# Optimization experiments

Measured on AMD Instinct MI355X. Metric: run time of the kernel, lower is better.

The kernel has to match this reference:

```python
import jax, jax.numpy as jnp
import numpy as np

V, E, H, O, L = 32000, 512, 512, 32, 2
B, T = 64, 512


def setup_inputs() -> dict:
    key = jax.random.key(0)
    ks = jax.random.split(key, 10)
    s = 0.02
    x = jax.random.randint(ks[0], (B, T), 0, V, dtype=jnp.int64)
    seq_lens = jax.random.randint(ks[1], (B,), 1, T + 1, dtype=jnp.int64)
    emb = jax.random.normal(ks[2], (V, E), dtype=jnp.float32) * s
    Whx = jax.random.normal(ks[3], (L, H, E), dtype=jnp.float32) * s  # [out,in] like nn.Linear
    Whh = jax.random.normal(ks[4], (L, H, H), dtype=jnp.float32) * s
    b_h = jnp.zeros((L, H), dtype=jnp.float32)
    Wyh = jax.random.normal(ks[5], (L, H, H), dtype=jnp.float32) * s
    b_y = jnp.zeros((L, H), dtype=jnp.float32)
    Wf = jax.random.normal(ks[6], (O, H), dtype=jnp.float32) * s
    bf = jnp.zeros((O,), dtype=jnp.float32)
    return {"x": x, "sequence_lengths": seq_lens, "emb": emb, "Whx": Whx,
            "Whh": Whh, "b_h": b_h, "Wyh": Wyh, "b_y": b_y, "Wf": Wf, "bf": bf}


def reference(x, sequence_lengths, emb, Whx, Whh, b_h, Wyh, b_y, Wf, bf):
    Bsz, Tlen = x.shape
    x_emb = emb[x]                      # [B,T,E]
    xs = jnp.swapaxes(x_emb, 0, 1)      # time-major [T,B,E]
    h0 = jnp.zeros((L, Bsz, H), dtype=x_emb.dtype)

    def step(h, xt):
        inp = xt
        hs = []
        for l in range(L):
            hl = jnp.tanh(inp @ Whx[l].T + h[l] @ Whh[l].T + b_h[l])
            hs.append(hl)
            inp = hl
        # only the last layer's y is kept by the original loop
        y = inp @ Wyh[L - 1].T + b_y[L - 1]
        return jnp.stack(hs), y

    _, outputs = jax.lax.scan(step, h0, xs)     # outputs: [T,B,H]
    outputs = jnp.swapaxes(outputs, 0, 1)       # [B,T,H]
    idx = sequence_lengths - 1                  # last valid timestep per example
    final_hidden = outputs[jnp.arange(Bsz), idx]  # [B,H]
    return final_hidden @ Wf.T + bf             # [B,O]
```

## Files before the change

kernel.cpp:

```cpp
#include <hip/hip_runtime.h>

namespace {
constexpr int E_ = 512;
constexpr int H_ = 512;
constexpr int O_ = 32;
constexpr int B_ = 64;
constexpr int T_ = 512;
constexpr int RING = 8;
constexpr int FPAD = 16;
constexpr size_t H0_OFF   = 0;
constexpr size_t H1_OFF   = (size_t)RING * B_ * H_;
constexpr size_t HF_OFF   = 2 * H1_OFF;
constexpr size_t FLAG_OFF = HF_OFF + (size_t)B_ * H_;
constexpr size_t FLAG_UINTS = 8u * 32u * FPAD;
constexpr size_t WS_REQUIRED = (FLAG_OFF + FLAG_UINTS) * 4;
}

typedef float f32x4 __attribute__((ext_vector_type(4)));

__device__ __forceinline__ void coh_ld2k(const float* p, f32x4& a, f32x4& b) {
    asm volatile(
        "global_load_dwordx4 %0, %2, off sc0 sc1\n\t"
        "global_load_dwordx4 %1, %2, off offset:1024 sc0 sc1\n\t"
        "s_waitcnt vmcnt(0)"
        : "=&v"(a), "=&v"(b) : "v"(p) : "memory");
}
__device__ __forceinline__ void coh_ld4k(const float* p, const float* q,
                                         f32x4& a, f32x4& b, f32x4& c, f32x4& d) {
    asm volatile(
        "global_load_dwordx4 %0, %4, off sc0 sc1\n\t"
        "global_load_dwordx4 %1, %4, off offset:1024 sc0 sc1\n\t"
        "global_load_dwordx4 %2, %5, off sc0 sc1\n\t"
        "global_load_dwordx4 %3, %5, off offset:1024 sc0 sc1\n\t"
        "s_waitcnt vmcnt(0)"
        : "=&v"(a), "=&v"(b), "=&v"(c), "=&v"(d) : "v"(p), "v"(q) : "memory");
}
__device__ __forceinline__ unsigned flag_poll(const unsigned* p) {
    unsigned v;
    asm volatile("global_load_dword %0, %1, off sc0 sc1\n\ts_waitcnt vmcnt(0)"
                 : "=&v"(v) : "v"(p) : "memory");
    return v;
}
__device__ __forceinline__ void coh_store_u(float* p, unsigned v) {
    asm volatile("global_store_dword %0, %1, off sc0 sc1" :: "v"(p), "v"(v) : "memory");
}
__device__ __forceinline__ void flag_store(unsigned* p, unsigned v) {
    asm volatile("global_store_dword %0, %1, off sc0 sc1" :: "v"(p), "v"(v) : "memory");
}

__device__ __forceinline__ float fast_tanh(float x) {
    float e = __builtin_amdgcn_exp2f(x * 2.885390081777927f);
    return 1.0f - 2.0f * __builtin_amdgcn_rcpf(e + 1.0f);
}

__device__ __forceinline__ float reduce4(const float v[4], int lane) {
    float a[2];
#pragma unroll
    for (int j = 0; j < 2; ++j) {
        const int sel = lane & 1;
        const float mine = sel ? v[2 * j + 1] : v[2 * j];
        const float send = sel ? v[2 * j] : v[2 * j + 1];
        a[j] = mine + __shfl_xor(send, 1, 64);
    }
    const int sel = (lane >> 1) & 1;
    const float mine = sel ? a[1] : a[0];
    const float send = sel ? a[0] : a[1];
    float s = mine + __shfl_xor(send, 2, 64);
    s += __shfl_xor(s, 4, 64);
    s += __shfl_xor(s, 8, 64);
    s += __shfl_xor(s, 16, 64);
    s += __shfl_xor(s, 32, 64);
    return s;
}

__global__ __launch_bounds__(512, 4) void rnn_pipe11(
    const int* __restrict__ x, const int* __restrict__ seq_lens,
    const float* __restrict__ emb,
    const float* __restrict__ Whx, const float* __restrict__ Whh,
    const float* __restrict__ b_h,
    float* __restrict__ h0_ring, float* __restrict__ h1_ring,
    float* __restrict__ h1_final, unsigned* __restrict__ flags)
{
    const int bid   = blockIdx.x;
    const int layer = bid >> 8;
    const int g     = (bid >> 5) & 7;
    const int c     = bid & 31;
    const int tid   = threadIdx.x;
    const int wid   = tid >> 6;
    const int lane  = tid & 63;
    const int we    = wid >> 2;
    const int wr    = wid & 3;
    const int rowbase = c * 16 + wr * 4;
    const int eg0   = g * 8 + we * 4;

    __shared__ float smem[12288];
    float* const sxA = smem;
    float* const sxB = smem + 4096;
    float* const sh  = smem + 8192;
    float* const sh1 = smem;

    const float* WxL = Whx + (size_t)layer * H_ * E_;
    const float* WhL = Whh + (size_t)layer * H_ * H_;
    f32x4 wx0[4], wx1[4], wh0[4], wh1[4];
#pragma unroll
    for (int r = 0; r < 4; ++r) {
        const int row = rowbase + r;
        wx0[r] = *(const f32x4*)(WxL + (size_t)row * E_ + (lane << 2));
        wx1[r] = *(const f32x4*)(WxL + (size_t)row * E_ + 256 + (lane << 2));
        wh0[r] = *(const f32x4*)(WhL + (size_t)row * H_ + (lane << 2));
        wh1[r] = *(const f32x4*)(WhL + (size_t)row * H_ + 256 + (lane << 2));
    }
    const float bias = b_h[layer * H_ + rowbase + (lane & 3)];

    int sl4[4];
#pragma unroll
    for (int q = 0; q < 4; ++q) sl4[q] = seq_lens[eg0 + q];
    int Tg = 1;
#pragma unroll
    for (int j = 0; j < 8; ++j) {
        const int s = seq_lens[g * 8 + j];
        Tg = s > Tg ? s : Tg;
    }

    unsigned* const myflag = flags + ((size_t)(g * 32 + c)) * FPAD;
    const unsigned* const bp = flags + ((size_t)(g * 32 + (lane & 31))) * FPAD;

    const int se  = wid;
    const int seg = g * 8 + se;

    long budget = 1l << 22;

    if (layer == 0) {
        {
            const int tok = x[(size_t)seg * T_];
            *(f32x4*)&sxA[(se << 9) + (lane << 2)] =
                *(const f32x4*)(emb + ((size_t)tok << 9) + (lane << 2));
            *(f32x4*)&sxA[(se << 9) + 256 + (lane << 2)] =
                *(const f32x4*)(emb + ((size_t)tok << 9) + 256 + (lane << 2));
        }
        __syncthreads();

        for (int t = 0; t < Tg; ++t) {
            const int cur = t & 1, slot = t & 7, pslot = (t - 1) & 7;
            float* const sxc = cur ? sxB : sxA;
            float* const sxn = cur ? sxA : sxB;
            const unsigned em_prev = (((t - 1) >> 3) & 1) ? 0xFFFFFFFFu : 0u;
            const unsigned em_cur  = ((t >> 3) & 1) ? 0xFFFFFFFFu : 0u;

            if (wid == 0 && t >= RING) {
                const int tgt = t - 7;
                for (;;) {
                    const unsigned v = flag_poll(bp);
                    const bool bad = (lane < 32) && ((int)v < tgt);
                    if (!__any(bad)) break;
                    if (--budget < 0) break;
                }
            }

            if (t > 0) {
                const float* src = h0_ring + (((size_t)pslot << 6) + seg) * 512 + (lane << 2);
                f32x4 da, db;
                for (;;) {
                    f32x4 a, b;
                    coh_ld2k(src, a, b);
                    unsigned o = 0;
#pragma unroll
                    for (int m = 0; m < 4; ++m) {
                        unsigned u = __float_as_uint(a[m]) ^ em_prev; o |= u; da[m] = __uint_as_float(u);
                        unsigned w = __float_as_uint(b[m]) ^ em_prev; o |= w; db[m] = __uint_as_float(w);
                    }
                    if (!__any((o >> 30) & 1)) break;
                    if (--budget < 0) break;
                }
                *(f32x4*)&sh[(se << 9) + (lane << 2)] = da;
                *(f32x4*)&sh[(se << 9) + 256 + (lane << 2)] = db;
            } else {
                f32x4 z = 0;
                *(f32x4*)&sh[(se << 9) + (lane << 2)] = z;
                *(f32x4*)&sh[(se << 9) + 256 + (lane << 2)] = z;
            }
            f32x4 px0, px1;
            const bool havepf = (t + 1 < Tg);
            if (havepf) {
                const int tok = x[(size_t)seg * T_ + t + 1];
                px0 = *(const f32x4*)(emb + ((size_t)tok << 9) + (lane << 2));
                px1 = *(const f32x4*)(emb + ((size_t)tok << 9) + 256 + (lane << 2));
            }
            __syncthreads();

#pragma unroll
            for (int q = 0; q < 4; ++q) {
                unsigned uenc = em_cur;
                if (t < sl4[q]) {
                    const int el = (we << 2) + q;
                    const f32x4 lx0 = *(const f32x4*)&sxc[(el << 9) + (lane << 2)];
                    const f32x4 lx1 = *(const f32x4*)&sxc[(el << 9) + 256 + (lane << 2)];
                    const f32x4 h0a = *(const f32x4*)&sh[(el << 9) + (lane << 2)];
                    const f32x4 h0b = *(const f32x4*)&sh[(el << 9) + 256 + (lane << 2)];
                    float vv[4];
#pragma unroll
                    for (int r = 0; r < 4; ++r) {
                        float s = wx0[r][0] * lx0[0];
                        s = fmaf(wx0[r][1], lx0[1], s);
                        s = fmaf(wx0[r][2], lx0[2], s);
                        s = fmaf(wx0[r][3], lx0[3], s);
                        s = fmaf(wx1[r][0], lx1[0], s);
                        s = fmaf(wx1[r][1], lx1[1], s);
                        s = fmaf(wx1[r][2], lx1[2], s);
                        s = fmaf(wx1[r][3], lx1[3], s);
                        s = fmaf(wh0[r][0], h0a[0], s);
                        s = fmaf(wh0[r][1], h0a[1], s);
                        s = fmaf(wh0[r][2], h0a[2], s);
                        s = fmaf(wh0[r][3], h0a[3], s);
                        s = fmaf(wh1[r][0], h0b[0], s);
                        s = fmaf(wh1[r][1], h0b[1], s);
                        s = fmaf(wh1[r][2], h0b[2], s);
                        s = fmaf(wh1[r][3], h0b[3], s);
                        vv[r] = s;
                    }
                    const float sum = reduce4(vv, lane);
                    const float hv = fast_tanh(sum + bias);
                    uenc = __float_as_uint(hv) ^ em_cur;
                }
                if (lane < 4)
                    coh_store_u(h0_ring + (((size_t)slot << 6) + eg0 + q) * 512 + rowbase + lane, uenc);
            }
            if (havepf) {
                *(f32x4*)&sxn[(se << 9) + (lane << 2)] = px0;
                *(f32x4*)&sxn[(se << 9) + 256 + (lane << 2)] = px1;
            }
            __syncthreads();
        }
    } else {
        for (int t = 0; t < Tg; ++t) {
            const int slot = t & 7, pslot = (t - 1) & 7;
            const unsigned em0 = ((t >> 3) & 1) ? 0xFFFFFFFFu : 0u;
            const unsigned em1 = (((t - 1) >> 3) & 1) ? 0xFFFFFFFFu : 0u;

            const float* p0 = h0_ring + (((size_t)slot << 6) + seg) * 512 + (lane << 2);
            if (t > 0) {
                const float* p1 = h1_ring + (((size_t)pslot << 6) + seg) * 512 + (lane << 2);
                f32x4 d0a, d0b, d1a, d1b;
                for (;;) {
                    f32x4 a, b, c2, d2;
                    coh_ld4k(p0, p1, a, b, c2, d2);
                    unsigned o = 0;
#pragma unroll
                    for (int m = 0; m < 4; ++m) {
                        unsigned u0 = __float_as_uint(a[m])  ^ em0; o |= u0; d0a[m] = __uint_as_float(u0);
                        unsigned u1 = __float_as_uint(b[m])  ^ em0; o |= u1; d0b[m] = __uint_as_float(u1);
                        unsigned u2 = __float_as_uint(c2[m]) ^ em1; o |= u2; d1a[m] = __uint_as_float(u2);
                        unsigned u3 = __float_as_uint(d2[m]) ^ em1; o |= u3; d1b[m] = __uint_as_float(u3);
                    }
                    if (!__any((o >> 30) & 1)) break;
                    if (--budget < 0) break;
                }
                *(f32x4*)&sh[(se << 9) + (lane << 2)] = d0a;
                *(f32x4*)&sh[(se << 9) + 256 + (lane << 2)] = d0b;
                *(f32x4*)&sh1[(se << 9) + (lane << 2)] = d1a;
                *(f32x4*)&sh1[(se << 9) + 256 + (lane << 2)] = d1b;
            } else {
                f32x4 d0a, d0b;
                for (;;) {
                    f32x4 a, b;
                    coh_ld2k(p0, a, b);
                    unsigned o = 0;
#pragma unroll
                    for (int m = 0; m < 4; ++m) {
                        unsigned u0 = __float_as_uint(a[m]) ^ em0; o |= u0; d0a[m] = __uint_as_float(u0);
                        unsigned u1 = __float_as_uint(b[m]) ^ em0; o |= u1; d0b[m] = __uint_as_float(u1);
                    }
                    if (!__any((o >> 30) & 1)) break;
                    if (--budget < 0) break;
                }
                *(f32x4*)&sh[(se << 9) + (lane << 2)] = d0a;
                *(f32x4*)&sh[(se << 9) + 256 + (lane << 2)] = d0b;
                f32x4 z = 0;
                *(f32x4*)&sh1[(se << 9) + (lane << 2)] = z;
                *(f32x4*)&sh1[(se << 9) + 256 + (lane << 2)] = z;
            }
            __syncthreads();
            if (tid == 0) flag_store(myflag, (unsigned)(t + 1));

#pragma unroll
            for (int q = 0; q < 4; ++q) {
                unsigned uenc = em0;
                const bool live = (t < sl4[q]);
                float hv = 0.f;
                if (live) {
                    const int el = (we << 2) + q;
                    const f32x4 xa = *(const f32x4*)&sh[(el << 9) + (lane << 2)];
                    const f32x4 xb = *(const f32x4*)&sh[(el << 9) + 256 + (lane << 2)];
                    const f32x4 ha = *(const f32x4*)&sh1[(el << 9) + (lane << 2)];
                    const f32x4 hb = *(const f32x4*)&sh1[(el << 9) + 256 + (lane << 2)];
                    float vv[4];
#pragma unroll
                    for (int r = 0; r < 4; ++r) {
                        float s = wx0[r][0] * xa[0];
                        s = fmaf(wx0[r][1], xa[1], s);
                        s = fmaf(wx0[r][2], xa[2], s);
                        s = fmaf(wx0[r][3], xa[3], s);
                        s = fmaf(wx1[r][0], xb[0], s);
                        s = fmaf(wx1[r][1], xb[1], s);
                        s = fmaf(wx1[r][2], xb[2], s);
                        s = fmaf(wx1[r][3], xb[3], s);
                        s = fmaf(wh0[r][0], ha[0], s);
                        s = fmaf(wh0[r][1], ha[1], s);
                        s = fmaf(wh0[r][2], ha[2], s);
                        s = fmaf(wh0[r][3], ha[3], s);
                        s = fmaf(wh1[r][0], hb[0], s);
                        s = fmaf(wh1[r][1], hb[1], s);
                        s = fmaf(wh1[r][2], hb[2], s);
                        s = fmaf(wh1[r][3], hb[3], s);
                        vv[r] = s;
                    }
                    const float sum = reduce4(vv, lane);
                    hv = fast_tanh(sum + bias);
                    uenc = __float_as_uint(hv) ^ em0;
                }
                if (lane < 4) {
                    coh_store_u(h1_ring + (((size_t)slot << 6) + eg0 + q) * 512 + rowbase + lane, uenc);
                    if (live && t == sl4[q] - 1)
                        h1_final[((size_t)(eg0 + q) << 9) + rowbase + lane] = hv;
                }
            }
            __syncthreads();
        }
    }
}

__device__ __forceinline__ float dot4(float4 a, float4 b) {
    return fmaf(a.x, b.x, fmaf(a.y, b.y, fmaf(a.z, b.z, a.w * b.w)));
}
__device__ __forceinline__ float wave_reduce(float acc) {
#pragma unroll
    for (int off = 32; off > 0; off >>= 1) acc += __shfl_down(acc, off, 64);
    return acc;
}

__global__ __launch_bounds__(512) void head_kernel(
    const float* __restrict__ h1f, const float* __restrict__ Wyh,
    const float* __restrict__ b_y, const float* __restrict__ Wf,
    const float* __restrict__ bf, float* __restrict__ out)
{
    const int e = blockIdx.x;
    const int tid = threadIdx.x, wid = tid >> 6, lane = tid & 63;
    const int k0 = lane << 3;
    __shared__ float sh[H_];
    __shared__ float sy[H_];
    sh[tid] = h1f[(size_t)e * H_ + tid];
    __syncthreads();
    const float4 hA = *(const float4*)&sh[k0];
    const float4 hB = *(const float4*)&sh[k0 + 4];
    const float* Wy1 = Wyh + H_ * H_;
#pragma unroll 4
    for (int rr = 0; rr < 64; ++rr) {
        const int row = (wid << 6) + rr;
        float acc = wave_reduce(dot4(*(const float4*)&Wy1[(size_t)row * H_ + k0], hA) +
                                dot4(*(const float4*)&Wy1[(size_t)row * H_ + k0 + 4], hB));
        if (lane == 0) sy[row] = acc + b_y[H_ + row];
    }
    __syncthreads();
    const float4 yA = *(const float4*)&sy[k0];
    const float4 yB = *(const float4*)&sy[k0 + 4];
#pragma unroll
    for (int rr = 0; rr < 4; ++rr) {
        const int o = (wid << 2) + rr;
        float acc = wave_reduce(dot4(*(const float4*)&Wf[(size_t)o * H_ + k0], yA) +
                                dot4(*(const float4*)&Wf[(size_t)o * H_ + k0 + 4], yB));
        if (lane == 0) out[(size_t)e * O_ + o] = acc + bf[o];
    }
}

__global__ __launch_bounds__(1024, 1) void rnn_fused_fb(
    const int* __restrict__ x, const int* __restrict__ seq_lens,
    const float* __restrict__ emb, const float* __restrict__ Whx,
    const float* __restrict__ Whh, const float* __restrict__ b_h,
    const float* __restrict__ Wyh, const float* __restrict__ b_y,
    const float* __restrict__ Wf, const float* __restrict__ bf,
    float* __restrict__ out)
{
    const int b = blockIdx.x, tid = threadIdx.x;
    const int wave = tid >> 6, lane = tid & 63, k0 = lane << 3;
    __shared__ float s_inp[E_];
    __shared__ float s_h0[2][H_];
    __shared__ float s_h1[2][H_];
    __shared__ float s_y[H_];
    if (tid < H_) { s_h0[0][tid]=0.f; s_h0[1][tid]=0.f; s_h1[0][tid]=0.f; s_h1[1][tid]=0.f; }
    const int Tb = seq_lens[b];
    const float* Whx0 = Whx; const float* Whx1 = Whx + H_*E_;
    const float* Whh0 = Whh; const float* Whh1 = Whh + H_*H_;
    for (int t = 0; t < Tb; ++t) {
        const int cur = t & 1, prv = cur ^ 1;
        if (tid < E_) { const int tok = x[b*T_+t]; s_inp[tid] = emb[(size_t)tok*E_+tid]; }
        __syncthreads();
        const float4 iA = *(const float4*)&s_inp[k0], iB = *(const float4*)&s_inp[k0+4];
        const float4 pA = *(const float4*)&s_h0[prv][k0], pB = *(const float4*)&s_h0[prv][k0+4];
#pragma unroll 4
        for (int r = 0; r < 32; ++r) {
            const int i = (wave<<5)+r;
            float acc = dot4(*(const float4*)&Whx0[i*E_+k0], iA) + dot4(*(const float4*)&Whx0[i*E_+k0+4], iB)
                      + dot4(*(const float4*)&Whh0[i*H_+k0], pA) + dot4(*(const float4*)&Whh0[i*H_+k0+4], pB);
            acc = wave_reduce(acc);
            if (lane == 0) s_h0[cur][i] = tanhf(acc + b_h[i]);
        }
        __syncthreads();
        const float4 cA = *(const float4*)&s_h0[cur][k0], cB = *(const float4*)&s_h0[cur][k0+4];
        const float4 qA = *(const float4*)&s_h1[prv][k0], qB = *(const float4*)&s_h1[prv][k0+4];
#pragma unroll 4
        for (int r = 0; r < 32; ++r) {
            const int i = (wave<<5)+r;
            float acc = dot4(*(const float4*)&Whx1[i*E_+k0], cA) + dot4(*(const float4*)&Whx1[i*E_+k0+4], cB)
                      + dot4(*(const float4*)&Whh1[i*H_+k0], qA) + dot4(*(const float4*)&Whh1[i*H_+k0+4], qB);
            acc = wave_reduce(acc);
            if (lane == 0) s_h1[cur][i] = tanhf(acc + b_h[H_+i]);
        }
        __syncthreads();
    }
    const int lastb = (Tb-1) & 1;
    const float4 hA = *(const float4*)&s_h1[lastb][k0], hB = *(const float4*)&s_h1[lastb][k0+4];
    const float* Wy1 = Wyh + H_*H_;
#pragma unroll 4
    for (int r = 0; r < 32; ++r) {
        const int i = (wave<<5)+r;
        float acc = wave_reduce(dot4(*(const float4*)&Wy1[i*H_+k0], hA) + dot4(*(const float4*)&Wy1[i*H_+k0+4], hB));
        if (lane == 0) s_y[i] = acc + b_y[H_+i];
    }
    __syncthreads();
    const float4 yA = *(const float4*)&s_y[k0], yB = *(const float4*)&s_y[k0+4];
    if (wave < 8) {
#pragma unroll
        for (int r = 0; r < 4; ++r) {
            const int o = (wave<<2)+r;
            float acc = wave_reduce(dot4(*(const float4*)&Wf[o*H_+k0], yA) + dot4(*(const float4*)&Wf[o*H_+k0+4], yB));
            if (lane == 0) out[b*O_+o] = acc + bf[o];
        }
    }
}

extern "C" void kernel_launch(void* const* d_in, const int* in_sizes, int n_in,
                              void* d_out, int out_size, void* d_ws, size_t ws_size,
                              hipStream_t stream) {
    const int*   x    = (const int*)d_in[0];
    const int*   sl   = (const int*)d_in[1];
    const float* emb  = (const float*)d_in[2];
    const float* Whx  = (const float*)d_in[3];
    const float* Whh  = (const float*)d_in[4];
    const float* b_h  = (const float*)d_in[5];
    const float* Wyh  = (const float*)d_in[6];
    const float* b_y  = (const float*)d_in[7];
    const float* Wf   = (const float*)d_in[8];
    const float* bf   = (const float*)d_in[9];
    float* out = (float*)d_out;

    if (ws_size < WS_REQUIRED) {
        rnn_fused_fb<<<B_, 1024, 0, stream>>>(x, sl, emb, Whx, Whh, b_h, Wyh, b_y, Wf, bf, out);
        return;
    }

    float* ws_f = (float*)d_ws;
    float* h0_ring = ws_f + H0_OFF;
    float* h1_ring = ws_f + H1_OFF;
    float* h1f     = ws_f + HF_OFF;
    unsigned* flags = (unsigned*)(ws_f + FLAG_OFF);

    hipMemsetAsync(h0_ring, 0xFF, 2 * H1_OFF * sizeof(float), stream);
    hipMemsetAsync(flags, 0, FLAG_UINTS * sizeof(unsigned), stream);
    rnn_pipe11<<<512, 512, 0, stream>>>(x, sl, emb, Whx, Whh, b_h,
                                        h0_ring, h1_ring, h1f, flags);
    head_kernel<<<B_, 512, 0, stream>>>(h1f, Wyh, b_y, Wf, bf, out);
}
```

Baseline: 1.941 ms.

## Sort batch by sequence length so groups share similar trip counts

Adds a small rank kernel that computes a permutation of batch elements sorted by descending sequence length. The recurrent kernel then assigns sorted examples to groups of eight, so each group's loop bound (the max length in the group) tracks its members closely and short groups exit early. This removes timesteps that were computed only because one long sequence sat in an otherwise short group. It costs an extra tiny kernel launch and an indirect lookup for tokens and final-state writes.

```diff
diff --git a/kernel.cpp b/kernel.cpp
--- a/kernel.cpp
+++ b/kernel.cpp
@@ -13,7 +13,8 @@
 constexpr size_t HF_OFF   = 2 * H1_OFF;
 constexpr size_t FLAG_OFF = HF_OFF + (size_t)B_ * H_;
 constexpr size_t FLAG_UINTS = 8u * 32u * FPAD;
-constexpr size_t WS_REQUIRED = (FLAG_OFF + FLAG_UINTS) * 4;
+constexpr size_t PERM_OFF = FLAG_OFF + FLAG_UINTS;
+constexpr size_t WS_REQUIRED = (PERM_OFF + 64) * 4;
 }
 
 typedef float f32x4 __attribute__((ext_vector_type(4)));
@@ -73,13 +74,25 @@
     return s;
 }
 
-__global__ __launch_bounds__(512, 4) void rnn_pipe11(
+__global__ void rank_kernel(const int* __restrict__ sl, int* __restrict__ perm) {
+    const int e = threadIdx.x;
+    const int my = sl[e];
+    int rank = 0;
+    for (int j = 0; j < B_; ++j) {
+        const int o = sl[j];
+        rank += (o > my) || (o == my && j < e);
+    }
+    perm[rank] = e;
+}
+
+__global__ __launch_bounds__(512, 4) void rnn_pipe12(
     const int* __restrict__ x, const int* __restrict__ seq_lens,
     const float* __restrict__ emb,
     const float* __restrict__ Whx, const float* __restrict__ Whh,
     const float* __restrict__ b_h,
     float* __restrict__ h0_ring, float* __restrict__ h1_ring,
-    float* __restrict__ h1_final, unsigned* __restrict__ flags)
+    float* __restrict__ h1_final, unsigned* __restrict__ flags,
+    const int* __restrict__ perm)
 {
     const int bid   = blockIdx.x;
     const int layer = bid >> 8;
@@ -112,13 +125,16 @@
     }
     const float bias = b_h[layer * H_ + rowbase + (lane & 3)];
 
-    int sl4[4];
-#pragma unroll
-    for (int q = 0; q < 4; ++q) sl4[q] = seq_lens[eg0 + q];
+    int pe[4], sl4[4];
+#pragma unroll
+    for (int q = 0; q < 4; ++q) {
+        pe[q]  = perm[eg0 + q];
+        sl4[q] = seq_lens[pe[q]];
+    }
     int Tg = 1;
 #pragma unroll
     for (int j = 0; j < 8; ++j) {
-        const int s = seq_lens[g * 8 + j];
+        const int s = seq_lens[perm[g * 8 + j]];
         Tg = s > Tg ? s : Tg;
     }
 
@@ -127,12 +143,13 @@
 
     const int se  = wid;
     const int seg = g * 8 + se;
+    const int pseg = perm[seg];
 
     long budget = 1l << 22;
 
     if (layer == 0) {
         {
-            const int tok = x[(size_t)seg * T_];
+            const int tok = x[(size_t)pseg * T_];
             *(f32x4*)&sxA[(se << 9) + (lane << 2)] =
                 *(const f32x4*)(emb + ((size_t)tok << 9) + (lane << 2));
             *(f32x4*)&sxA[(se << 9) + 256 + (lane << 2)] =
@@ -182,7 +199,7 @@
             f32x4 px0, px1;
             const bool havepf = (t + 1 < Tg);
             if (havepf) {
-                const int tok = x[(size_t)seg * T_ + t + 1];
+                const int tok = x[(size_t)pseg * T_ + t + 1];
                 px0 = *(const f32x4*)(emb + ((size_t)tok << 9) + (lane << 2));
                 px1 = *(const f32x4*)(emb + ((size_t)tok << 9) + 256 + (lane << 2));
             }
@@ -321,7 +338,7 @@
                 if (lane < 4) {
                     coh_store_u(h1_ring + (((size_t)slot << 6) + eg0 + q) * 512 + rowbase + lane, uenc);
                     if (live && t == sl4[q] - 1)
-                        h1_final[((size_t)(eg0 + q) << 9) + rowbase + lane] = hv;
+                        h1_final[((size_t)pe[q] << 9) + rowbase + lane] = hv;
                 }
             }
             __syncthreads();
@@ -463,10 +480,12 @@
     float* h1_ring = ws_f + H1_OFF;
     float* h1f     = ws_f + HF_OFF;
     unsigned* flags = (unsigned*)(ws_f + FLAG_OFF);
+    int* perm = (int*)(ws_f + PERM_OFF);
 
     hipMemsetAsync(h0_ring, 0xFF, 2 * H1_OFF * sizeof(float), stream);
     hipMemsetAsync(flags, 0, FLAG_UINTS * sizeof(unsigned), stream);
-    rnn_pipe11<<<512, 512, 0, stream>>>(x, sl, emb, Whx, Whh, b_h,
-                                        h0_ring, h1_ring, h1f, flags);
+    rank_kernel<<<1, 64, 0, stream>>>(sl, perm);
+    rnn_pipe12<<<512, 512, 0, stream>>>(x, sl, emb, Whx, Whh, b_h,
+                                        h0_ring, h1_ring, h1f, flags, perm);
     head_kernel<<<B_, 512, 0, stream>>>(h1f, Wyh, b_y, Wf, bf, out);
 }
```

Result: slower. 2.054 ms (+5.8%).
